# Kernel tuning notes

Measured on AMD Instinct MI355X. Metric: run time of the kernel, lower is better.

The kernel has to match this reference:

```python
import jax, jax.numpy as jnp
import numpy as np

K = 8192   # codebook_size
D = 256    # latent_dim
COMMITMENT_COST = 0.25


def setup_inputs() -> dict:
    key = jax.random.key(0)
    kx, kw = jax.random.split(key)
    x = jax.random.normal(kx, (8, 4096, D), dtype=jnp.float32)
    # nn.init.uniform_(weight, -1/K, 1/K)
    weight = jax.random.uniform(kw, (K, D), dtype=jnp.float32,
                                minval=-1.0 / K, maxval=1.0 / K)
    return {"x": x, "weight": weight}


def reference(x, weight):
    sg = jax.lax.stop_gradient
    orig_shape = x.shape
    x_flat = x.reshape(-1, D)                      # [N, D]
    # squared euclidean distances; argmin identical to cdist argmin
    x_sq = jnp.sum(x_flat * x_flat, axis=-1, keepdims=True)      # [N, 1]
    w_sq = jnp.sum(weight * weight, axis=-1)                     # [K]
    dist2 = x_sq - 2.0 * (x_flat @ weight.T) + w_sq              # [N, K]
    indices = jnp.argmin(dist2, axis=1)                          # [N]
    quantized = jnp.take(weight, indices, axis=0).reshape(orig_shape)
    # eval / non-EMA branch of the torch module
    commitment_loss = jnp.mean((x - sg(quantized)) ** 2) * COMMITMENT_COST
    codebook_loss = jnp.mean((quantized - sg(x)) ** 2)
    total = commitment_loss + codebook_loss
    # straight-through estimator
    quantized_st = x + sg(quantized - x)
    indices_out = indices.reshape(orig_shape[:-1])
    return quantized_st, indices_out, commitment_loss, codebook_loss, total
```

## Files before the change

kernel.cpp:

```cpp
#include <hip/hip_runtime.h>

#define K_CB   8192
#define D_DIM  256
#define N_ROWS 32768
#define Q_ELEMS (N_ROWS * D_DIM)

#define M_FLAG 1.3e-4f
#define M_CAND 1.3e-4f
#define CAP    32

typedef __bf16 bf16x8 __attribute__((ext_vector_type(8)));
typedef float  f32x16 __attribute__((ext_vector_type(16)));

#define ASYNC_COPY16(gp, lp)                                              \
    __builtin_amdgcn_global_load_lds(                                     \
        (const __attribute__((address_space(1))) unsigned int*)(gp),      \
        (__attribute__((address_space(3))) unsigned int*)(lp), 16, 0, 0)


__device__ inline ushort f2bf(float f) {
    unsigned u = __float_as_uint(f);
    unsigned r = u + 0x7FFFu + ((u >> 16) & 1u);
    return (ushort)(r >> 16);
}

__device__ inline uint4 pack8(float4 a, float4 b) {
    uint4 o;
    o.x = (unsigned)f2bf(a.x) | ((unsigned)f2bf(a.y) << 16);
    o.y = (unsigned)f2bf(a.z) | ((unsigned)f2bf(a.w) << 16);
    o.z = (unsigned)f2bf(b.x) | ((unsigned)f2bf(b.y) << 16);
    o.w = (unsigned)f2bf(b.z) | ((unsigned)f2bf(b.w) << 16);
    return o;
}

__global__ void wsq_wbf_kernel(const float* __restrict__ w, float* __restrict__ wsq,
                               ushort* __restrict__ wbf) {
    int wave = threadIdx.x >> 6, lane = threadIdx.x & 63;
    int row = blockIdx.x * 4 + wave;
    float4 v = reinterpret_cast<const float4*>(w)[(size_t)row * 64 + lane];
    uint2 o;
    o.x = (unsigned)f2bf(-2.0f * v.x) | ((unsigned)f2bf(-2.0f * v.y) << 16);
    o.y = (unsigned)f2bf(-2.0f * v.z) | ((unsigned)f2bf(-2.0f * v.w) << 16);
    int c = row & 127, tile = row >> 7;
    int s = lane >> 1, hq = lane & 1;
    size_t dst = (size_t)tile * 65536 + (size_t)c * 512 + (size_t)((s ^ (c & 7)) * 16) + hq * 8;
    *reinterpret_cast<uint2*>((char*)wbf + dst) = o;
    double sq = (double)v.x * v.x + (double)v.y * v.y + (double)v.z * v.z + (double)v.w * v.w;
    #pragma unroll
    for (int off = 32; off > 0; off >>= 1) sq += __shfl_down(sq, off, 64);
    if (lane == 0) wsq[row] = (float)sq;
}

__global__ void sqx_kernel(const float* __restrict__ m, float* __restrict__ out) {
    int wave = threadIdx.x >> 6, lane = threadIdx.x & 63;
    int row = blockIdx.x * 4 + wave;
    float4 v = reinterpret_cast<const float4*>(m)[(size_t)row * 64 + lane];
    double s = (double)v.x * v.x + (double)v.y * v.y + (double)v.z * v.z + (double)v.w * v.w;
    #pragma unroll
    for (int off = 32; off > 0; off >>= 1) s += __shfl_down(s, off, 64);
    if (lane == 0) out[row] = (float)s;
}

__global__ __launch_bounds__(256, 2) void pass1_kernel(
        const float* __restrict__ x, const ushort* __restrict__ wbf,
        const float* __restrict__ wsq, float* __restrict__ idx_out,
        float* __restrict__ rowmin, int* __restrict__ flags,
        unsigned* __restrict__ flag_count, int* __restrict__ candcnt) {
    __shared__ __align__(16) ushort wt[128 * 256];

    const int t = threadIdx.x;
    const int lane = t & 63, ln31 = lane & 31, h = lane >> 5;
    const int wv = t >> 6, rs = wv & 1, cs = wv >> 1;
    const int r0 = blockIdx.x * 64;

    const int arow = r0 + rs * 32 + ln31;
    const float4* xr = reinterpret_cast<const float4*>(x) + (size_t)arow * 64;
    bf16x8 afr[16];
    #pragma unroll
    for (int kk = 0; kk < 16; ++kk)
        afr[kk] = __builtin_bit_cast(bf16x8, pack8(xr[kk * 4 + h * 2], xr[kk * 4 + h * 2 + 1]));

    float b1[16], b2[16];
    #pragma unroll
    for (int r = 0; r < 16; ++r) { b1[r] = 3.4e38f; b2[r] = 3.4e38f; }

    const int col0 = cs * 64 + ln31, c70 = col0 & 7;
    const char* gW = (const char*)wbf + (size_t)wv * 16384 + (size_t)lane * 16;
    char* lW = (char*)wt + wv * 16384;

    for (int tile = 0; tile < 64; ++tile) {
        __syncthreads();
        const char* gt = gW + (size_t)tile * 65536;
        #pragma unroll
        for (int i = 0; i < 16; ++i)
            ASYNC_COPY16(gt + i * 1024, lW + i * 1024);
        __syncthreads();

        int kb = tile * 128 + col0;
        float wsk0 = wsq[kb], wsk1 = wsq[kb + 32];

        f32x16 acc0 = {0,0,0,0,0,0,0,0,0,0,0,0,0,0,0,0};
        f32x16 acc1 = {0,0,0,0,0,0,0,0,0,0,0,0,0,0,0,0};
        #pragma unroll
        for (int kk = 0; kk < 16; ++kk) {
            int s = kk * 2 + h;
            bf16x8 bf0 = *reinterpret_cast<const bf16x8*>(&wt[col0 * 256 + ((s ^ c70) * 8)]);
            bf16x8 bf1 = *reinterpret_cast<const bf16x8*>(&wt[(col0 + 32) * 256 + ((s ^ c70) * 8)]);
            acc0 = __builtin_amdgcn_mfma_f32_32x32x16_bf16(afr[kk], bf0, acc0, 0, 0, 0);
            acc1 = __builtin_amdgcn_mfma_f32_32x32x16_bf16(afr[kk], bf1, acc1, 0, 0, 0);
        }

        #pragma unroll
        for (int r = 0; r < 16; ++r) {
            float s0 = acc0[r] + wsk0;
            float p0 = __uint_as_float((__float_as_uint(s0) & 0xFFFFE000u) | (unsigned)kb);
            b2[r] = __builtin_amdgcn_fmed3f(p0, b1[r], b2[r]);
            b1[r] = fminf(p0, b1[r]);
            float s1 = acc1[r] + wsk1;
            float p1 = __uint_as_float((__float_as_uint(s1) & 0xFFFFE000u) | (unsigned)(kb + 32));
            b2[r] = __builtin_amdgcn_fmed3f(p1, b1[r], b2[r]);
            b1[r] = fminf(p1, b1[r]);
        }
    }

    __syncthreads();
    float* sb1 = reinterpret_cast<float*>(wt);
    float* sb2 = sb1 + 4096;
    #pragma unroll
    for (int r = 0; r < 16; ++r) {
        int rl = rs * 32 + (r & 3) + 8 * (r >> 2) + 4 * h;
        sb1[rl * 64 + cs * 32 + ln31] = b1[r];
        sb2[rl * 64 + cs * 32 + ln31] = b2[r];
    }
    __syncthreads();
    if (t < 64) {
        float B1 = 3.4e38f, B2 = 3.4e38f;
        for (int c = 0; c < 64; ++c) {
            float a1 = sb1[t * 64 + c], a2 = sb2[t * 64 + c];
            float nb2 = fminf(fmaxf(B1, a1), fminf(B2, a2));
            B1 = fminf(B1, a1);
            B2 = nb2;
        }
        int row = r0 + t;
        idx_out[row] = (float)(__float_as_uint(B1) & 0x1FFFu);
        rowmin[row]  = B1;
        candcnt[row] = 0;
        if (B2 - B1 <= M_FLAG) {
            unsigned pos = atomicAdd(flag_count, 1u);
            if (pos < N_ROWS) flags[pos] = row;
        }
    }
}

__global__ __launch_bounds__(256, 2) void fixup_kernel(
        const float* __restrict__ x, const ushort* __restrict__ wbf,
        const float* __restrict__ wsq, const float* __restrict__ rowmin,
        const int* __restrict__ flags, const unsigned* __restrict__ flag_count,
        int* __restrict__ candcnt, int* __restrict__ cands) {
    __shared__ __align__(16) ushort wt[128 * 256];
    __shared__ int   sh_rows[64];
    __shared__ float sh_thr[64];

    const int t = threadIdx.x;
    const int lane = t & 63, ln31 = lane & 31, h = lane >> 5;
    const int wv = t >> 6, rs = wv & 1, cs = wv >> 1;

    unsigned cu = flag_count[0];
    int cnt = cu > N_ROWS ? N_ROWS : (int)cu;
    int nunits = ((cnt + 63) >> 6) * 8;

    for (int u = blockIdx.x; u < nunits; u += 512) {
        int ksp  = u & 7;
        int base = (u >> 3) * 64;
        int nrows = cnt - base; if (nrows > 64) nrows = 64;

        __syncthreads();
        if (t < 64) {
            int valid = (t < nrows);
            int gr = flags[base + (valid ? t : 0)];
            sh_rows[t] = gr;
            sh_thr[t]  = valid ? rowmin[gr] + M_CAND : -3.4e38f;
        }
        __syncthreads();

        int arow = sh_rows[rs * 32 + ln31];
        const float4* xr = reinterpret_cast<const float4*>(x) + (size_t)arow * 64;
        bf16x8 afr[16];
        #pragma unroll
        for (int kk = 0; kk < 16; ++kk)
            afr[kk] = __builtin_bit_cast(bf16x8, pack8(xr[kk * 4 + h * 2], xr[kk * 4 + h * 2 + 1]));
        float thr_r[16];
        int   rl_r[16];
        #pragma unroll
        for (int r = 0; r < 16; ++r) {
            rl_r[r]  = rs * 32 + (r & 3) + 8 * (r >> 2) + 4 * h;
            thr_r[r] = sh_thr[rl_r[r]];
        }

        const int col0 = cs * 64 + ln31, c70 = col0 & 7;
        char* lW = (char*)wt + wv * 16384;

        for (int tile = 0; tile < 8; ++tile) {
            int ct0 = ksp * 1024 + tile * 128;
            __syncthreads();
            const char* gt = (const char*)wbf + ((size_t)ct0 << 9)
                           + (size_t)wv * 16384 + (size_t)lane * 16;
            #pragma unroll
            for (int i = 0; i < 16; ++i)
                ASYNC_COPY16(gt + i * 1024, lW + i * 1024);
            __syncthreads();

            float wsk0 = wsq[ct0 + col0], wsk1 = wsq[ct0 + col0 + 32];
            f32x16 acc0 = {0,0,0,0,0,0,0,0,0,0,0,0,0,0,0,0};
            f32x16 acc1 = {0,0,0,0,0,0,0,0,0,0,0,0,0,0,0,0};
            #pragma unroll
            for (int kk = 0; kk < 16; ++kk) {
                int s = kk * 2 + h;
                bf16x8 bf0 = *reinterpret_cast<const bf16x8*>(&wt[col0 * 256 + ((s ^ c70) * 8)]);
                bf16x8 bf1 = *reinterpret_cast<const bf16x8*>(&wt[(col0 + 32) * 256 + ((s ^ c70) * 8)]);
                acc0 = __builtin_amdgcn_mfma_f32_32x32x16_bf16(afr[kk], bf0, acc0, 0, 0, 0);
                acc1 = __builtin_amdgcn_mfma_f32_32x32x16_bf16(afr[kk], bf1, acc1, 0, 0, 0);
            }
            #pragma unroll
            for (int r = 0; r < 16; ++r) {
                float s0 = acc0[r] + wsk0;
                if (s0 <= thr_r[r]) {
                    int grow = sh_rows[rl_r[r]];
                    int pos = atomicAdd(&candcnt[grow], 1);
                    if (pos < CAP) cands[grow * CAP + pos] = ct0 + col0;
                }
                float s1 = acc1[r] + wsk1;
                if (s1 <= thr_r[r]) {
                    int grow = sh_rows[rl_r[r]];
                    int pos = atomicAdd(&candcnt[grow], 1);
                    if (pos < CAP) cands[grow * CAP + pos] = ct0 + col0 + 32;
                }
            }
        }
    }
}

__global__ __launch_bounds__(256) void rescore_kernel(
        const float* __restrict__ x, const float* __restrict__ w,
        const float* __restrict__ wsq, const float* __restrict__ xsq,
        const int* __restrict__ flags, const unsigned* __restrict__ flag_count,
        const int* __restrict__ candcnt, const int* __restrict__ cands,
        float* __restrict__ idx_out) {
    int wid  = (blockIdx.x * 256 + threadIdx.x) >> 6;
    int lane = threadIdx.x & 63;
    unsigned cu = flag_count[0];
    int cnt = (cu > N_ROWS) ? N_ROWS : (int)cu;

    for (int fi = wid; fi < cnt; fi += 1024) {
        int row = flags[fi];
        float4 xv = reinterpret_cast<const float4*>(x)[(size_t)row * 64 + lane];
        float Xs = xsq[row];
        int nc = candcnt[row]; if (nc > CAP) nc = CAP;
        float bq = 3.4e38f; int bk = -1;
        for (int c = 0; c < nc; ++c) {
            int k = cands[row * CAP + c];
            float4 wv = reinterpret_cast<const float4*>(w)[(size_t)k * 64 + lane];
            double d = (double)xv.x * wv.x + (double)xv.y * wv.y
                     + (double)xv.z * wv.z + (double)xv.w * wv.w;
            #pragma unroll
            for (int off = 1; off < 64; off <<= 1) d += __shfl_xor(d, off, 64);
            float XW = (float)d;
            float t3 = fmaf(-2.0f, XW, Xs);
            float qv = t3 + wsq[k];
            if (qv < bq || (qv == bq && k < bk) || bk < 0) { bq = qv; bk = k; }
        }
        if (lane == 0 && bk >= 0) idx_out[row] = (float)bk;
    }
}

__global__ __launch_bounds__(256) void gather_loss_kernel(
        const float* __restrict__ x, const float* __restrict__ w,
        const float* __restrict__ idx_f, float* __restrict__ out_q,
        float* __restrict__ accum) {
    const int nf4 = Q_ELEMS / 4;
    float lsum = 0.0f;
    for (int e = blockIdx.x * blockDim.x + threadIdx.x; e < nf4;
         e += gridDim.x * blockDim.x) {
        int row = e >> 6, d4 = e & 63;
        int k = (int)idx_f[row];
        float4 xv = reinterpret_cast<const float4*>(x)[e];
        float4 qv = reinterpret_cast<const float4*>(w)[(size_t)k * 64 + d4];
        float4 ov;
        ov.x = xv.x + (qv.x - xv.x);
        ov.y = xv.y + (qv.y - xv.y);
        ov.z = xv.z + (qv.z - xv.z);
        ov.w = xv.w + (qv.w - xv.w);
        reinterpret_cast<float4*>(out_q)[e] = ov;
        float dx = xv.x - qv.x, dy = xv.y - qv.y, dz = xv.z - qv.z, dw = xv.w - qv.w;
        lsum += dx * dx + dy * dy + dz * dz + dw * dw;
    }
    #pragma unroll
    for (int off = 32; off > 0; off >>= 1) lsum += __shfl_down(lsum, off, 64);
    __shared__ float ssum[4];
    if ((threadIdx.x & 63) == 0) ssum[threadIdx.x >> 6] = lsum;
    __syncthreads();
    if (threadIdx.x == 0)
        atomicAdd(accum, ssum[0] + ssum[1] + ssum[2] + ssum[3]);
}

__global__ void finalize_kernel(const float* __restrict__ accum,
                                float* __restrict__ out_tail) {
    float mse = accum[0] / (float)Q_ELEMS;
    float commit = 0.25f * mse;
    out_tail[0] = commit;
    out_tail[1] = mse;
    out_tail[2] = commit + mse;
}

extern "C" void kernel_launch(void* const* d_in, const int* in_sizes, int n_in,
                              void* d_out, int out_size, void* d_ws, size_t ws_size,
                              hipStream_t stream) {
    const float* x = (const float*)d_in[0];
    const float* w = (const float*)d_in[1];
    float* out = (float*)d_out;

    char* ws = (char*)d_ws;
    float*    Wsq        = (float*)ws;
    float*    Xsq        = (float*)(ws + 32768);
    float*    Rmin       = (float*)(ws + 163840);
    float*    accum      = (float*)(ws + 294912);
    unsigned* flag_count = (unsigned*)(ws + 294916);
    int*      flags      = (int*)(ws + 294920);
    int*      candcnt    = (int*)(ws + 425992);
    int*      cands      = (int*)(ws + 557064);
    ushort*   Wbf        = (ushort*)(ws + 4751376);

    hipMemsetAsync(ws + 294912, 0, 8, stream);
    wsq_wbf_kernel<<<K_CB / 4, 256, 0, stream>>>(w, Wsq, Wbf);
    sqx_kernel<<<N_ROWS / 4, 256, 0, stream>>>(x, Xsq);
    pass1_kernel<<<N_ROWS / 64, 256, 0, stream>>>(x, Wbf, Wsq, out + Q_ELEMS,
                                                  Rmin, flags, flag_count, candcnt);
    fixup_kernel<<<512, 256, 0, stream>>>(x, Wbf, Wsq, Rmin, flags, flag_count,
                                          candcnt, cands);
    rescore_kernel<<<256, 256, 0, stream>>>(x, w, Wsq, Xsq, flags, flag_count,
                                            candcnt, cands, out + Q_ELEMS);
    gather_loss_kernel<<<8192, 256, 0, stream>>>(x, w, out + Q_ELEMS, out, accum);
    finalize_kernel<<<1, 1, 0, stream>>>(accum, out + Q_ELEMS + N_ROWS);
}
```

Before: 449.5 us.

## Collect rescore candidates in pass1 and only run fixup on hard rows

Pass1 now scans the per-column best values of flagged rows, writes candidate code indices directly when each column holds at most one near-tie and the total fits in the cap, and sends only the remaining 'hard' rows to the fixup GEMM kernel. This is meant to avoid recomputing full codebook distances for most flagged rows. The shared-memory reduction buffers are padded to a stride of 65 to avoid bank conflicts, and the candidate cap drops from 32 to 16, which shrinks the workspace. The cost is a serial 64-column scan per flagged row in the pass1 epilogue and more rows falling back to the hard path when candidates overflow the smaller cap.

```diff
diff --git a/kernel.cpp b/kernel.cpp
--- a/kernel.cpp
+++ b/kernel.cpp
@@ -7,7 +7,7 @@
 
 #define M_FLAG 1.3e-4f
 #define M_CAND 1.3e-4f
-#define CAP    32
+#define CAP    16
 
 typedef __bf16 bf16x8 __attribute__((ext_vector_type(8)));
 typedef float  f32x16 __attribute__((ext_vector_type(16)));
@@ -65,7 +65,9 @@
         const float* __restrict__ x, const ushort* __restrict__ wbf,
         const float* __restrict__ wsq, float* __restrict__ idx_out,
         float* __restrict__ rowmin, int* __restrict__ flags,
-        unsigned* __restrict__ flag_count, int* __restrict__ candcnt) {
+        unsigned* __restrict__ flag_count, int* __restrict__ hard_flags,
+        unsigned* __restrict__ hard_count, int* __restrict__ candcnt,
+        int* __restrict__ cands) {
     __shared__ __align__(16) ushort wt[128 * 256];
 
     const int t = threadIdx.x;
@@ -125,18 +127,18 @@
 
     __syncthreads();
     float* sb1 = reinterpret_cast<float*>(wt);
-    float* sb2 = sb1 + 4096;
+    float* sb2 = sb1 + 4160;
     #pragma unroll
     for (int r = 0; r < 16; ++r) {
         int rl = rs * 32 + (r & 3) + 8 * (r >> 2) + 4 * h;
-        sb1[rl * 64 + cs * 32 + ln31] = b1[r];
-        sb2[rl * 64 + cs * 32 + ln31] = b2[r];
+        sb1[rl * 65 + cs * 32 + ln31] = b1[r];
+        sb2[rl * 65 + cs * 32 + ln31] = b2[r];
     }
     __syncthreads();
     if (t < 64) {
         float B1 = 3.4e38f, B2 = 3.4e38f;
         for (int c = 0; c < 64; ++c) {
-            float a1 = sb1[t * 64 + c], a2 = sb2[t * 64 + c];
+            float a1 = sb1[t * 65 + c], a2 = sb2[t * 65 + c];
             float nb2 = fminf(fmaxf(B1, a1), fminf(B2, a2));
             B1 = fminf(B1, a1);
             B2 = nb2;
@@ -144,18 +146,35 @@
         int row = r0 + t;
         idx_out[row] = (float)(__float_as_uint(B1) & 0x1FFFu);
         rowmin[row]  = B1;
-        candcnt[row] = 0;
+        int nc = 0;
         if (B2 - B1 <= M_FLAG) {
             unsigned pos = atomicAdd(flag_count, 1u);
             if (pos < N_ROWS) flags[pos] = row;
-        }
+            float T = B1 + M_CAND;
+            bool hard = false;
+            for (int c = 0; c < 64; ++c) {
+                float a1 = sb1[t * 65 + c];
+                if (a1 <= T) {
+                    if (nc < CAP) cands[row * CAP + nc] = (int)(__float_as_uint(a1) & 0x1FFFu);
+                    ++nc;
+                }
+                if (sb2[t * 65 + c] <= T) hard = true;
+            }
+            if (nc > CAP) hard = true;
+            if (hard) {
+                nc = 0;
+                unsigned hp = atomicAdd(hard_count, 1u);
+                if (hp < N_ROWS) hard_flags[hp] = row;
+            }
+        }
+        candcnt[row] = nc;
     }
 }
 
 __global__ __launch_bounds__(256, 2) void fixup_kernel(
         const float* __restrict__ x, const ushort* __restrict__ wbf,
         const float* __restrict__ wsq, const float* __restrict__ rowmin,
-        const int* __restrict__ flags, const unsigned* __restrict__ flag_count,
+        const int* __restrict__ hard_flags, const unsigned* __restrict__ hard_count,
         int* __restrict__ candcnt, int* __restrict__ cands) {
     __shared__ __align__(16) ushort wt[128 * 256];
     __shared__ int   sh_rows[64];
@@ -165,7 +184,7 @@
     const int lane = t & 63, ln31 = lane & 31, h = lane >> 5;
     const int wv = t >> 6, rs = wv & 1, cs = wv >> 1;
 
-    unsigned cu = flag_count[0];
+    unsigned cu = hard_count[0];
     int cnt = cu > N_ROWS ? N_ROWS : (int)cu;
     int nunits = ((cnt + 63) >> 6) * 8;
 
@@ -177,7 +196,7 @@
         __syncthreads();
         if (t < 64) {
             int valid = (t < nrows);
-            int gr = flags[base + (valid ? t : 0)];
+            int gr = hard_flags[base + (valid ? t : 0)];
             sh_rows[t] = gr;
             sh_thr[t]  = valid ? rowmin[gr] + M_CAND : -3.4e38f;
         }
@@ -325,17 +344,21 @@
     float*    Rmin       = (float*)(ws + 163840);
     float*    accum      = (float*)(ws + 294912);
     unsigned* flag_count = (unsigned*)(ws + 294916);
-    int*      flags      = (int*)(ws + 294920);
-    int*      candcnt    = (int*)(ws + 425992);
-    int*      cands      = (int*)(ws + 557064);
-    ushort*   Wbf        = (ushort*)(ws + 4751376);
-
-    hipMemsetAsync(ws + 294912, 0, 8, stream);
+    unsigned* hard_count = (unsigned*)(ws + 294920);
+    int*      flags      = (int*)(ws + 294924);
+    int*      hard_flags = (int*)(ws + 425996);
+    int*      candcnt    = (int*)(ws + 557068);
+    int*      cands      = (int*)(ws + 688140);
+    ushort*   Wbf        = (ushort*)(ws + 2785296);
+
+    hipMemsetAsync(ws + 294912, 0, 12, stream);
     wsq_wbf_kernel<<<K_CB / 4, 256, 0, stream>>>(w, Wsq, Wbf);
     sqx_kernel<<<N_ROWS / 4, 256, 0, stream>>>(x, Xsq);
     pass1_kernel<<<N_ROWS / 64, 256, 0, stream>>>(x, Wbf, Wsq, out + Q_ELEMS,
-                                                  Rmin, flags, flag_count, candcnt);
-    fixup_kernel<<<512, 256, 0, stream>>>(x, Wbf, Wsq, Rmin, flags, flag_count,
+                                                  Rmin, flags, flag_count,
+                                                  hard_flags, hard_count,
+                                                  candcnt, cands);
+    fixup_kernel<<<512, 256, 0, stream>>>(x, Wbf, Wsq, Rmin, hard_flags, hard_count,
                                           candcnt, cands);
     rescore_kernel<<<256, 256, 0, stream>>>(x, w, Wsq, Xsq, flags, flag_count,
                                             candcnt, cands, out + Q_ELEMS);
```

Result: faster. 412.3 us (-8.3%).
